# Kernel tuning notes

Measured on AMD Instinct MI355X. Metric: run time of the kernel, lower is better.

The kernel has to match this reference:

```python
import jax, jax.numpy as jnp
import numpy as np

EPS = 1e-5  # torch GroupNorm default
KNN_K = 16


def _knn_idx(Q, P, K):
    # Q:[B,Nq,3], P:[B,Np,3] -> idx [B,Nq,K], ascending squared distance
    d = (jnp.sum(Q * Q, -1)[:, :, None] + jnp.sum(P * P, -1)[:, None, :]
         - 2.0 * jnp.einsum('bqc,bkc->bqk', Q, P))
    _, idx = jax.lax.top_k(-d, K)
    return idx


def _gather_nbr(feat_bnc, idx_bqk):
    # feat:[B,Np,C], idx:[B,Nq,K] -> [B,Nq,K,C]  (knn_gather)
    return jax.vmap(lambda f, i: f[i])(feat_bnc, idx_bqk)


def _group_norm(x_bcnk, gamma, beta, num_groups=8):
    B, C, N, K = x_bcnk.shape
    G = min(num_groups, C)
    xg = x_bcnk.reshape(B, G, C // G, N, K)
    mu = xg.mean(axis=(2, 3, 4), keepdims=True)
    var = xg.var(axis=(2, 3, 4), keepdims=True)
    xn = ((xg - mu) / jnp.sqrt(var + EPS)).reshape(B, C, N, K)
    return xn * gamma[None, :, None, None] + beta[None, :, None, None]


def _edge_conv(Fq_bcn, Fk_bcn, Pq_b3n, Pk_b3n, k, W, gamma, beta):
    # EdgeConv: concat(x_j - x_i, x_i) -> conv1x1 -> GN -> ReLU -> max over K
    idx = _knn_idx(Pq_b3n.transpose(0, 2, 1), Pk_b3n.transpose(0, 2, 1), k)
    nbr = _gather_nbr(Fk_bcn.transpose(0, 2, 1), idx)          # [B,Nq,K,Cin]
    Fi = jnp.broadcast_to(Fq_bcn.transpose(0, 2, 1)[:, :, None, :], nbr.shape)
    pair = jnp.concatenate([nbr - Fi, Fi], axis=-1)            # [B,Nq,K,2Cin]
    out = jnp.einsum('oc,bnkc->bonk', W, pair)                 # conv 1x1, no bias
    out = _group_norm(out, gamma, beta)
    out = jax.nn.relu(out)
    return out.max(axis=-1)                                    # [B,Cout,Nq]


def _fps_idx(P_b3n, m):
    # Farthest point sampling starting at index 0 (pytorch3d default)
    def one(Pn3):
        d0 = jnp.sum((Pn3 - Pn3[0]) ** 2, -1)
        def step(dists, _):
            nxt = jnp.argmax(dists)
            d = jnp.sum((Pn3 - Pn3[nxt]) ** 2, -1)
            return jnp.minimum(dists, d), nxt
        _, idxs = jax.lax.scan(step, d0, None, length=m - 1)
        return jnp.concatenate([jnp.zeros((1,), jnp.int32), idxs.astype(jnp.int32)])
    return jax.vmap(one)(P_b3n.transpose(0, 2, 1))


def _gather_bcn(x_bcn, idx_bm):
    return jax.vmap(lambda x, i: x[:, i])(x_bcn, idx_bm)


def setup_inputs() -> dict:
    key = jax.random.key(0)
    ks = jax.random.split(key, 8)
    B, N = 2, 8192
    def w(k, shape, s=0.1):
        return jax.random.normal(k, shape, jnp.float32) * s
    return {
        'xyz': jax.random.normal(ks[0], (B, 3, N), jnp.float32),
        'stem_w': w(ks[1], (8, 3)), 'stem_b': jnp.zeros((8,), jnp.float32),
        'w1': w(ks[2], (32, 16)),  'g1': jnp.ones((32,), jnp.float32),  'b1': jnp.zeros((32,), jnp.float32),
        'w2': w(ks[3], (64, 64)),  'g2': jnp.ones((64,), jnp.float32),  'b2': jnp.zeros((64,), jnp.float32),
        'w3': w(ks[4], (64, 128)), 'g3': jnp.ones((64,), jnp.float32),  'b3': jnp.zeros((64,), jnp.float32),
        'w4': w(ks[5], (128, 128)),'g4': jnp.ones((128,), jnp.float32), 'b4': jnp.zeros((128,), jnp.float32),
    }


def reference(xyz, stem_w, stem_b, w1, g1, b1, w2, g2, b2, w3, g3, b3, w4, g4, b4):
    K = KNN_K
    P0 = xyz                                                     # [B,3,N0]
    F0 = jnp.einsum('oc,bcn->bon', stem_w, xyz) + stem_b[None, :, None]
    F0a = _edge_conv(F0, F0, P0, P0, K, w1, g1, b1)              # [B,32,N0]
    N0 = P0.shape[2]
    N1 = max(1, N0 // 4)
    idx1 = _fps_idx(P0, N1)
    P1 = _gather_bcn(P0, idx1)
    F1sk = _gather_bcn(F0a, idx1)
    F1a = _edge_conv(F1sk, F0a, P1, P0, K, w2, g2, b2)           # [B,64,N1]
    N2 = max(1, N1 // 4)
    idx2 = _fps_idx(P1, N2)
    P2 = _gather_bcn(P1, idx2)
    F2sk = _gather_bcn(F1a, idx2)
    F2mid = _edge_conv(F2sk, F1a, P2, P1, K, w3, g3, b3)         # [B,64,N2]
    F2a = _edge_conv(F2mid, F1a, P2, P1, K, w4, g4, b4)          # [B,128,N2]
    return (P0, F0a, P1, F1a, P2, F2a)
```

## Files before the change

kernel.cpp:

```cpp
#include <hip/hip_runtime.h>
#include <math.h>

typedef unsigned long long ull;

__global__ __launch_bounds__(256) void stem_fused(const float* __restrict__ xyz,
    const float* __restrict__ w, const float* __restrict__ bias,
    float* __restrict__ F0, float* __restrict__ P0o, int N){
  int id = blockIdx.x*256 + threadIdx.x;
  int n = id % N; int b = id / N;
  float x = xyz[((size_t)b*3+0)*N+n];
  float y = xyz[((size_t)b*3+1)*N+n];
  float z = xyz[((size_t)b*3+2)*N+n];
  P0o[((size_t)b*3+0)*N+n] = x;
  P0o[((size_t)b*3+1)*N+n] = y;
  P0o[((size_t)b*3+2)*N+n] = z;
  #pragma unroll
  for (int o=0;o<8;o++){
    float v = fmaf(w[o*3+0],x, fmaf(w[o*3+1],y, fmaf(w[o*3+2],z, bias[o])));
    F0[((size_t)b*8+o)*N+n] = v;
  }
}

__global__ __launch_bounds__(256) void knn_fused(
    const float* __restrict__ Pq, const float* __restrict__ Pp,
    int* __restrict__ idxk, int Nq, int Np){
  __shared__ float4 tile[4][256];
  __shared__ float  pd[16][4][64];
  __shared__ int    pi[16][4][64];
  int t = threadIdx.x, w = t>>6, l = t&63;
  int b = blockIdx.y;
  int qn = blockIdx.x*64 + l;
  const float* Pqb = Pq + (size_t)b*3*Nq;
  const float* Ppb = Pp + (size_t)b*3*Np;
  float qx = Pqb[qn], qy = Pqb[Nq+qn], qz = Pqb[2*Nq+qn];
  float qq = __fadd_rn(__fadd_rn(__fmul_rn(qx,qx),__fmul_rn(qy,qy)),__fmul_rn(qz,qz));

  float dl[16]; int il[16];
  #pragma unroll
  for (int u=0;u<16;u++){ dl[u]=INFINITY; il[u]=-1; }
  float maxd = INFINITY; int maxslot = 0;

  int CANDS = Np >> 2;
  int c0 = w*CANDS;
  for (int tb=0; tb<CANDS; tb+=256){
    __syncthreads();
    #pragma unroll
    for (int k=0;k<4;k++){
      int p = c0 + tb + k*64 + l;
      float px = Ppb[p], py = Ppb[Np+p], pz = Ppb[2*Np+p];
      float pp = __fadd_rn(__fadd_rn(__fmul_rn(px,px),__fmul_rn(py,py)),__fmul_rn(pz,pz));
      tile[w][k*64+l] = make_float4(px,py,pz,pp);
    }
    __syncthreads();
    for (int j=0;j<256;j++){
      float4 c = tile[w][j];
      float dot = __fadd_rn(__fadd_rn(__fmul_rn(qx,c.x),__fmul_rn(qy,c.y)),__fmul_rn(qz,c.z));
      float dc  = __fsub_rn(__fadd_rn(qq,c.w), __fmul_rn(2.0f,dot));
      if (dc < maxd){
        int pidx = c0 + tb + j;
        #pragma unroll
        for (int u=0;u<16;u++){ bool sel=(maxslot==u); dl[u]=sel?dc:dl[u]; il[u]=sel?pidx:il[u]; }
        maxd = dl[0]; maxslot = 0;
        #pragma unroll
        for (int u=1;u<16;u++){ bool g=(dl[u]>maxd); maxd=g?dl[u]:maxd; maxslot=g?u:maxslot; }
      }
    }
  }
  #pragma unroll
  for (int u=0;u<16;u++){ pd[u][w][l]=dl[u]; pi[u][w][l]=il[u]; }
  __syncthreads();
  if (t < 64){
    int q = t;
    float mdl[16]; int mil[16];
    #pragma unroll
    for (int u=0;u<16;u++){ mdl[u]=INFINITY; mil[u]=0x7fffffff; }
    float mmaxd = INFINITY; int mmaxi = 0x7fffffff; int mslot = 0;
    for (int s=0;s<4;s++){
      #pragma unroll
      for (int u=0;u<16;u++){
        float d = pd[u][s][q]; int ii = pi[u][s][q];
        bool better = (d < mmaxd) || (d == mmaxd && ii < mmaxi);
        if (better){
          #pragma unroll
          for (int v=0;v<16;v++){ bool sel=(mslot==v); mdl[v]=sel?d:mdl[v]; mil[v]=sel?ii:mil[v]; }
          mmaxd = mdl[0]; mmaxi = mil[0]; mslot = 0;
          #pragma unroll
          for (int v=1;v<16;v++){
            bool g = (mdl[v]>mmaxd) || (mdl[v]==mmaxd && mil[v]>mmaxi);
            mmaxd=g?mdl[v]:mmaxd; mmaxi=g?mil[v]:mmaxi; mslot=g?v:mslot;
          }
        }
      }
    }
    #pragma unroll
    for (int u=0;u<16;u++)
      idxk[((size_t)b*Nq + blockIdx.x*64 + q)*16 + u] = mil[u];
  }
}

template<int CIN, int COUT>
__global__ __launch_bounds__(1024) void edge_conv_pre(
    const float* __restrict__ Fk, const float* __restrict__ Fi,
    const int* __restrict__ idx, const float* __restrict__ W,
    float* __restrict__ pre, float* __restrict__ partS,
    float* __restrict__ partQ, int pstride, int Nq, int Np){
  constexpr int C2  = 2*CIN;
  constexpr int PAD = C2 + 4;
  constexpr int TO  = (COUT <= 64) ? COUT : 64;
  constexpr int OP  = COUT / TO;
  constexpr int CPG = COUT/8;
  constexpr int WPG = CPG/4;
  extern __shared__ float sm[];
  float* Wl = sm;
  float* Pl = sm + COUT*PAD;
  int t = threadIdx.x;
  int n = blockIdx.x, b = blockIdx.y;
  for (int e=t; e<COUT*C2; e += blockDim.x){
    int o=e/C2, c=e%C2; Wl[o*PAD+c] = W[e];
  }
  const int* idxn = idx + ((size_t)b*Nq + n)*16;
  for (int e=t; e<16*C2; e += blockDim.x){
    int k = e/C2, c = e%C2;
    int cc = (c < CIN) ? c : (c-CIN);
    float fi = Fi[((size_t)b*CIN + cc)*Nq + n];
    float v;
    if (c < CIN){ int nb = idxn[k]; v = Fk[((size_t)b*CIN + c)*Np + nb] - fi; }
    else v = fi;
    Pl[k*PAD+c] = v;
  }
  __syncthreads();
  int k = t & 15, o0 = t >> 4;
  float accv[OP];
  #pragma unroll
  for (int op=0; op<OP; op++){
    int o = o0 + op*TO;
    float acc = 0.f;
    #pragma unroll
    for (int c=0;c<C2;c+=4){
      float4 wv = *(const float4*)&Wl[o*PAD+c];
      float4 pv = *(const float4*)&Pl[k*PAD+c];
      acc = fmaf(wv.x,pv.x,acc); acc = fmaf(wv.y,pv.y,acc);
      acc = fmaf(wv.z,pv.z,acc); acc = fmaf(wv.w,pv.w,acc);
    }
    accv[op] = acc;
    pre[(((size_t)b*COUT + o)*Nq + n)*16 + k] = acc;
  }
  int w = t>>6;
  #pragma unroll
  for (int op=0; op<OP; op++){
    float s1 = accv[op], s2 = accv[op]*accv[op];
    #pragma unroll
    for (int off=32; off>=1; off>>=1){ s1 += __shfl_down(s1,off); s2 += __shfl_down(s2,off); }
    if ((t&63)==0){
      int o = o0 + op*TO;
      int g = o / CPG;
      int slot = n*WPG + (w % WPG);
      partS[((size_t)(b*8+g))*pstride + slot] = s1;
      partQ[((size_t)(b*8+g))*pstride + slot] = s2;
    }
  }
}

__global__ __launch_bounds__(256) void gn_combine(const float* __restrict__ partS,
    const float* __restrict__ partQ, float2* __restrict__ stats,
    int nslot, int pstride, double cnt){
  int bg = blockIdx.x, t = threadIdx.x;
  const float* ps = partS + (size_t)bg*pstride;
  const float* pq = partQ + (size_t)bg*pstride;
  double s=0.0, q=0.0;
  for (int i=t; i<nslot; i+=256){ s += (double)ps[i]; q += (double)pq[i]; }
  #pragma unroll
  for (int off=32; off>=1; off>>=1){ s += __shfl_down(s,off); q += __shfl_down(q,off); }
  __shared__ double ls[4], lq[4];
  int wid = t>>6;
  if ((t&63)==0){ ls[wid]=s; lq[wid]=q; }
  __syncthreads();
  if (t==0){
    double S=ls[0]+ls[1]+ls[2]+ls[3], Q=lq[0]+lq[1]+lq[2]+lq[3];
    double mu = S/cnt;
    double var = Q/cnt - mu*mu;
    stats[bg] = make_float2((float)mu, (float)(1.0/sqrt(var+1e-5)));
  }
}

template<int COUT>
__global__ __launch_bounds__(256) void gn_apply(const float* __restrict__ pre,
    const float2* __restrict__ stats, const float* __restrict__ gamma,
    const float* __restrict__ beta, float* __restrict__ outF, int Nq){
  int id = blockIdx.x*256 + threadIdx.x;
  int o = (id/Nq)%COUT; int b = id/(Nq*COUT);
  int g = o/(COUT/8);
  float2 st = stats[b*8+g];
  float muf = st.x, rstd = st.y;
  float ga=gamma[o], be=beta[o];
  const float4* p = (const float4*)(pre + (size_t)id*16);
  float m = 0.f;
  #pragma unroll
  for (int q=0;q<4;q++){
    float4 v = p[q];
    m = fmaxf(m, fmaf((v.x-muf)*rstd, ga, be));
    m = fmaxf(m, fmaf((v.y-muf)*rstd, ga, be));
    m = fmaxf(m, fmaf((v.z-muf)*rstd, ga, be));
    m = fmaxf(m, fmaf((v.w-muf)*rstd, ga, be));
  }
  outF[id] = m;
}

template<int COUT>
__global__ __launch_bounds__(1024) void gn_fused(const float* __restrict__ pre,
    const float* __restrict__ gamma, const float* __restrict__ beta,
    float* __restrict__ outF, int Nq){
  constexpr int CPG = COUT/8;
  int g = blockIdx.x, b = blockIdx.y, t = threadIdx.x;
  size_t base = (((size_t)b*COUT + g*CPG)*(size_t)Nq)*16;
  const float* p = pre + base;
  int len = CPG*Nq*16;
  double s=0.0, sq=0.0;
  for (int i = t*4; i < len; i += 4096){
    float4 v = *(const float4*)(p+i);
    s += (double)v.x; sq = fma((double)v.x,(double)v.x,sq);
    s += (double)v.y; sq = fma((double)v.y,(double)v.y,sq);
    s += (double)v.z; sq = fma((double)v.z,(double)v.z,sq);
    s += (double)v.w; sq = fma((double)v.w,(double)v.w,sq);
  }
  #pragma unroll
  for (int off=32; off>=1; off>>=1){ s += __shfl_down(s, off); sq += __shfl_down(sq, off); }
  __shared__ double ls[16], lq[16];
  __shared__ float stats[2];
  int wid = t>>6;
  if ((t&63)==0){ ls[wid]=s; lq[wid]=sq; }
  __syncthreads();
  if (t==0){
    double S=0.0, Q=0.0;
    #pragma unroll
    for (int w=0;w<16;w++){ S+=ls[w]; Q+=lq[w]; }
    double cnt = (double)CPG*(double)Nq*16.0;
    double mu  = S/cnt;
    double var = Q/cnt - mu*mu;
    stats[0] = (float)mu;
    stats[1] = (float)(1.0/sqrt(var+1e-5));
  }
  __syncthreads();
  float muf = stats[0], rstd = stats[1];
  int outs = CPG*Nq;
  for (int e=t; e<outs; e+=1024){
    int ol = e/Nq, n = e - ol*Nq;
    int o = g*CPG + ol;
    float ga = gamma[o], be = beta[o];
    const float4* pp = (const float4*)(p + (size_t)e*16);
    float m = 0.f;
    #pragma unroll
    for (int q=0;q<4;q++){
      float4 v = pp[q];
      m = fmaxf(m, fmaf((v.x-muf)*rstd, ga, be));
      m = fmaxf(m, fmaf((v.y-muf)*rstd, ga, be));
      m = fmaxf(m, fmaf((v.z-muf)*rstd, ga, be));
      m = fmaxf(m, fmaf((v.w-muf)*rstd, ga, be));
    }
    outF[((size_t)b*COUT + o)*Nq + n] = m;
  }
}

template<int CTRL>
__device__ __forceinline__ float dpp_maxf(float x){
  int y = __builtin_amdgcn_update_dpp(0, __float_as_int(x), CTRL, 0xf, 0xf, true);
  return fmaxf(x, __int_as_float(y));
}

template<int PPT, int BLK, int M>
__global__ __launch_bounds__(BLK, 2) void fps_kernel(const float* __restrict__ P,
    int* __restrict__ idx_out){
  constexpr int N  = PPT*BLK;
  constexpr int NW = BLK/64;
  extern __shared__ __align__(16) float sm[];
  float* lx = sm; float* ly = sm+N; float* lz = sm+2*N;
  ull* wk = (ull*)(sm + 3*N);
  int b = blockIdx.x, t = threadIdx.x;
  const float* Pb = P + (size_t)b*3*N;
  for (int i=t; i<N; i+=BLK){ lx[i]=Pb[i]; ly[i]=Pb[N+i]; lz[i]=Pb[2*N+i]; }
  __syncthreads();
  float px[PPT], py[PPT], pz[PPT], dist[PPT];
  #pragma unroll
  for (int j=0;j<PPT;j++){ int p=t*PPT+j; px[j]=lx[p]; py[j]=ly[p]; pz[j]=lz[p]; }
  #pragma unroll
  for (int j=0;j<PPT;j++){
    asm volatile("" : "+v"(px[j]), "+v"(py[j]), "+v"(pz[j]));
  }
  float sx = lx[0], sy = ly[0], sz = lz[0];
  float bd = -1.f; int bj = 0;
  #pragma unroll
  for (int j=0;j<PPT;j++){
    float dx=__fsub_rn(px[j],sx), dy=__fsub_rn(py[j],sy), dz=__fsub_rn(pz[j],sz);
    float dd=__fadd_rn(__fadd_rn(__fmul_rn(dx,dx),__fmul_rn(dy,dy)),__fmul_rn(dz,dz));
    dist[j]=dd;
    bool c = dd > bd; bd = c?dd:bd; bj = c?j:bj;
  }
  int pbest = t*PPT + bj;
  if (t==0) idx_out[(size_t)b*M] = 0;
  int wid = t>>6, lane = t&63, par = 0;
  for (int i=1;i<M;i++){
    float r = bd;
    r = dpp_maxf<0x111>(r); r = dpp_maxf<0x112>(r);
    r = dpp_maxf<0x114>(r); r = dpp_maxf<0x118>(r);
    r = dpp_maxf<0x142>(r); r = dpp_maxf<0x143>(r);
    float wmax = __int_as_float(__builtin_amdgcn_readlane(__float_as_int(r), 63));
    ull msk = __ballot(bd == wmax);
    int srcl = __ffsll(msk) - 1;
    int wp = __builtin_amdgcn_readlane(pbest, srcl);
    if (lane==0)
      wk[par*NW + wid] = ((ull)__float_as_uint(wmax)<<32)
                       | (unsigned)(~(unsigned)wp);
    __syncthreads();
    ull best = wk[par*NW];
    #pragma unroll
    for (int w=1;w<NW;w++){ ull o = wk[par*NW+w]; best = (o>best)?o:best; }
    unsigned widx = ~(unsigned)best;
    if (t==0) idx_out[(size_t)b*M + i] = (int)widx;
    float nsx = lx[widx], nsy = ly[widx], nsz = lz[widx];
    par ^= 1;
    float nbd = -1.f; int nbj = 0;
    #pragma unroll
    for (int j=0;j<PPT;j++){
      float dx=__fsub_rn(px[j],nsx), dy=__fsub_rn(py[j],nsy), dz=__fsub_rn(pz[j],nsz);
      float dd=__fadd_rn(__fadd_rn(__fmul_rn(dx,dx),__fmul_rn(dy,dy)),__fmul_rn(dz,dz));
      float nd = fminf(dist[j], dd);
      dist[j] = nd;
      bool c = nd > nbd; nbd = c?nd:nbd; nbj = c?j:nbj;
    }
    bd = nbd; pbest = t*PPT + nbj;
  }
}

__global__ __launch_bounds__(256) void gather_fused(float* __restrict__ Pdst,
    const float* __restrict__ Psrc, float* __restrict__ Fdst,
    const float* __restrict__ Fsrc, const int* __restrict__ idxv,
    int CF, int Nsrc, int M){
  int per = (3+CF)*M;
  int total = 2*per;
  for (int id = blockIdx.x*256 + threadIdx.x; id < total; id += gridDim.x*256){
    int b = id/per, r = id%per, c = r/M, m = r%M;
    int sn = idxv[(size_t)b*M + m];
    if (c < 3)
      Pdst[((size_t)b*3+c)*M+m] = Psrc[((size_t)b*3+c)*Nsrc+sn];
    else {
      int cf = c-3;
      Fdst[((size_t)b*CF+cf)*M+m] = Fsrc[((size_t)b*CF+cf)*Nsrc+sn];
    }
  }
}

extern "C" void kernel_launch(void* const* d_in, const int* in_sizes, int n_in,
                              void* d_out, int out_size, void* d_ws, size_t ws_size,
                              hipStream_t stream) {
  const float* xyz    = (const float*)d_in[0];
  const float* stem_w = (const float*)d_in[1];
  const float* stem_b = (const float*)d_in[2];
  const float* w1 = (const float*)d_in[3];
  const float* g1 = (const float*)d_in[4];
  const float* b1 = (const float*)d_in[5];
  const float* w2 = (const float*)d_in[6];
  const float* g2 = (const float*)d_in[7];
  const float* b2 = (const float*)d_in[8];
  const float* w3 = (const float*)d_in[9];
  const float* g3 = (const float*)d_in[10];
  const float* b3 = (const float*)d_in[11];
  const float* w4 = (const float*)d_in[12];
  const float* g4 = (const float*)d_in[13];
  const float* b4 = (const float*)d_in[14];

  float* out = (float*)d_out;
  float* P0o  = out + 0;
  float* F0a  = out + 49152;
  float* P1o  = out + 573440;
  float* F1a  = out + 585728;
  float* P2o  = out + 847872;
  float* F2a  = out + 850944;

  char* ws = (char*)d_ws;
  float* F0     = (float*)(ws + 0);
  float* pre    = (float*)(ws + 524288);
  int*   idxk   = (int*)  (ws + 34078720);
  float2* stats = (float2*)(ws + 35127296);
  int*   idx1   = (int*)  (ws + 35127424);
  int*   idx2   = (int*)  (ws + 35143808);
  float* F1sk   = (float*)(ws + 35147904);
  float* F2sk   = (float*)(ws + 35672192);
  float* F2mid  = (float*)(ws + 35934336);
  float* pS1 = (float*)(ws + 35147904);
  float* pQ1 = (float*)(ws + 35672192);
  float* pS2 = (float*)(ws + 17825792);
  float* pQ2 = (float*)(ws + 18087936);

  size_t smem_c1 = (size_t)(32*20  + 16*20 )*4;
  size_t smem_c2 = (size_t)(64*68  + 16*68 )*4;
  size_t smem_c3 = (size_t)(64*132 + 16*132)*4;
  size_t smem_c4 = (size_t)(128*132+ 16*132)*4;
  size_t smem_f1 = (size_t)3*8192*4 + 256;
  size_t smem_f2 = (size_t)3*2048*4 + 256;

  stem_fused<<<64, 256, 0, stream>>>(xyz, stem_w, stem_b, F0, P0o, 8192);
  knn_fused<<<dim3(128,2), 256, 0, stream>>>(xyz, xyz, idxk, 8192, 8192);
  edge_conv_pre<8,32><<<dim3(8192,2), 512, smem_c1, stream>>>(F0, F0, idxk, w1, pre, pS1, pQ1, 8192, 8192, 8192);
  gn_combine<<<16, 256, 0, stream>>>(pS1, pQ1, stats, 8192, 8192, 524288.0);
  gn_apply<32><<<2048, 256, 0, stream>>>(pre, stats, g1, b1, F0a, 8192);

  fps_kernel<16,512,2048><<<2, 512, smem_f1, stream>>>(xyz, idx1);
  gather_fused<<<560, 256, 0, stream>>>(P1o, xyz, F1sk, F0a, idx1, 32, 8192, 2048);

  knn_fused<<<dim3(32,2), 256, 0, stream>>>(P1o, xyz, idxk, 2048, 8192);
  edge_conv_pre<32,64><<<dim3(2048,2), 1024, smem_c2, stream>>>(F0a, F1sk, idxk, w2, pre, pS2, pQ2, 4096, 2048, 8192);
  gn_combine<<<16, 256, 0, stream>>>(pS2, pQ2, stats, 4096, 4096, 262144.0);
  gn_apply<64><<<1024, 256, 0, stream>>>(pre, stats, g2, b2, F1a, 2048);

  fps_kernel<4,512,512><<<2, 512, smem_f2, stream>>>(P1o, idx2);
  gather_fused<<<268, 256, 0, stream>>>(P2o, P1o, F2sk, F1a, idx2, 64, 2048, 512);

  knn_fused<<<dim3(8,2), 256, 0, stream>>>(P2o, P1o, idxk, 512, 2048);
  edge_conv_pre<64,64><<<dim3(512,2), 1024, smem_c3, stream>>>(F1a, F2sk, idxk, w3, pre, pS2, pQ2, 4096, 512, 2048);
  gn_fused<64><<<dim3(8,2), 1024, 0, stream>>>(pre, g3, b3, F2mid, 512);

  edge_conv_pre<64,128><<<dim3(512,2), 1024, smem_c4, stream>>>(F1a, F2mid, idxk, w4, pre, pS2, pQ2, 4096, 512, 2048);
  gn_fused<128><<<dim3(8,2), 1024, 0, stream>>>(pre, g4, b4, F2a, 512);

  (void)in_sizes; (void)n_in; (void)out_size; (void)ws_size;
}
```

Measured before the change: 3.609 ms.

## Run FPS concurrently with stem and KNN in merged heterogeneous launches

Merges farthest-point sampling, the stem projection and the first-level KNN into one launch where block ids pick the role, and does the same for the second FPS with the second KNN. The serial FPS scan, which uses only two blocks, now runs alongside the parallel KNN work instead of after it. FPS now uses 256-thread blocks with twice the points per thread, which lengthens each block's serial loop. Every block of the merged kernels reserves the large FPS shared-memory allocation, which may limit KNN occupancy.

```diff
diff --git a/kernel.cpp b/kernel.cpp
--- a/kernel.cpp
+++ b/kernel.cpp
@@ -3,33 +3,83 @@
 
 typedef unsigned long long ull;
 
-__global__ __launch_bounds__(256) void stem_fused(const float* __restrict__ xyz,
-    const float* __restrict__ w, const float* __restrict__ bias,
-    float* __restrict__ F0, float* __restrict__ P0o, int N){
-  int id = blockIdx.x*256 + threadIdx.x;
-  int n = id % N; int b = id / N;
-  float x = xyz[((size_t)b*3+0)*N+n];
-  float y = xyz[((size_t)b*3+1)*N+n];
-  float z = xyz[((size_t)b*3+2)*N+n];
-  P0o[((size_t)b*3+0)*N+n] = x;
-  P0o[((size_t)b*3+1)*N+n] = y;
-  P0o[((size_t)b*3+2)*N+n] = z;
-  #pragma unroll
-  for (int o=0;o<8;o++){
-    float v = fmaf(w[o*3+0],x, fmaf(w[o*3+1],y, fmaf(w[o*3+2],z, bias[o])));
-    F0[((size_t)b*8+o)*N+n] = v;
-  }
-}
-
-__global__ __launch_bounds__(256) void knn_fused(
-    const float* __restrict__ Pq, const float* __restrict__ Pp,
-    int* __restrict__ idxk, int Nq, int Np){
-  __shared__ float4 tile[4][256];
-  __shared__ float  pd[16][4][64];
-  __shared__ int    pi[16][4][64];
+template<int CTRL>
+__device__ __forceinline__ float dpp_maxf(float x){
+  int y = __builtin_amdgcn_update_dpp(0, __float_as_int(x), CTRL, 0xf, 0xf, true);
+  return fmaxf(x, __int_as_float(y));
+}
+
+template<int PPT, int BLK, int M>
+__device__ void fps_body(const float* __restrict__ P, int* __restrict__ idx_out,
+                         int b, float* sm){
+  constexpr int N  = PPT*BLK;
+  constexpr int NW = BLK/64;
+  float* lx = sm; float* ly = sm+N; float* lz = sm+2*N;
+  ull* wk = (ull*)(sm + 3*N);
+  int t = threadIdx.x;
+  const float* Pb = P + (size_t)b*3*N;
+  for (int i=t; i<N; i+=BLK){ lx[i]=Pb[i]; ly[i]=Pb[N+i]; lz[i]=Pb[2*N+i]; }
+  __syncthreads();
+  float px[PPT], py[PPT], pz[PPT], dist[PPT];
+  #pragma unroll
+  for (int j=0;j<PPT;j++){ int p=t*PPT+j; px[j]=lx[p]; py[j]=ly[p]; pz[j]=lz[p]; }
+  #pragma unroll
+  for (int j=0;j<PPT;j++){
+    asm volatile("" : "+v"(px[j]), "+v"(py[j]), "+v"(pz[j]));
+  }
+  float sx = lx[0], sy = ly[0], sz = lz[0];
+  float bd = -1.f; int bj = 0;
+  #pragma unroll
+  for (int j=0;j<PPT;j++){
+    float dx=__fsub_rn(px[j],sx), dy=__fsub_rn(py[j],sy), dz=__fsub_rn(pz[j],sz);
+    float dd=__fadd_rn(__fadd_rn(__fmul_rn(dx,dx),__fmul_rn(dy,dy)),__fmul_rn(dz,dz));
+    dist[j]=dd;
+    bool c = dd > bd; bd = c?dd:bd; bj = c?j:bj;
+  }
+  int pbest = t*PPT + bj;
+  if (t==0) idx_out[(size_t)b*M] = 0;
+  int wid = t>>6, lane = t&63, par = 0;
+  for (int i=1;i<M;i++){
+    float r = bd;
+    r = dpp_maxf<0x111>(r); r = dpp_maxf<0x112>(r);
+    r = dpp_maxf<0x114>(r); r = dpp_maxf<0x118>(r);
+    r = dpp_maxf<0x142>(r); r = dpp_maxf<0x143>(r);
+    float wmax = __int_as_float(__builtin_amdgcn_readlane(__float_as_int(r), 63));
+    ull msk = __ballot(bd == wmax);
+    int srcl = __ffsll(msk) - 1;
+    int wp = __builtin_amdgcn_readlane(pbest, srcl);
+    if (lane==0)
+      wk[par*NW + wid] = ((ull)__float_as_uint(wmax)<<32)
+                       | (unsigned)(~(unsigned)wp);
+    __syncthreads();
+    ull best = wk[par*NW];
+    #pragma unroll
+    for (int w=1;w<NW;w++){ ull o = wk[par*NW+w]; best = (o>best)?o:best; }
+    unsigned widx = ~(unsigned)best;
+    if (t==0) idx_out[(size_t)b*M + i] = (int)widx;
+    float nsx = lx[widx], nsy = ly[widx], nsz = lz[widx];
+    par ^= 1;
+    float nbd = -1.f; int nbj = 0;
+    #pragma unroll
+    for (int j=0;j<PPT;j++){
+      float dx=__fsub_rn(px[j],nsx), dy=__fsub_rn(py[j],nsy), dz=__fsub_rn(pz[j],nsz);
+      float dd=__fadd_rn(__fadd_rn(__fmul_rn(dx,dx),__fmul_rn(dy,dy)),__fmul_rn(dz,dz));
+      float nd = fminf(dist[j], dd);
+      dist[j] = nd;
+      bool c = nd > nbd; nbd = c?nd:nbd; nbj = c?j:nbj;
+    }
+    bd = nbd; pbest = t*PPT + nbj;
+  }
+}
+
+__device__ void knn_body(const float* __restrict__ Pq, const float* __restrict__ Pp,
+                         int* __restrict__ idxk, int Nq, int Np, int qb, int b,
+                         float* smbase){
+  float4* tile = (float4*)smbase;
+  float*  pd   = smbase + 4096;
+  int*    pi   = (int*)(smbase + 8192);
   int t = threadIdx.x, w = t>>6, l = t&63;
-  int b = blockIdx.y;
-  int qn = blockIdx.x*64 + l;
+  int qn = qb*64 + l;
   const float* Pqb = Pq + (size_t)b*3*Nq;
   const float* Ppb = Pp + (size_t)b*3*Np;
   float qx = Pqb[qn], qy = Pqb[Nq+qn], qz = Pqb[2*Nq+qn];
@@ -49,11 +99,11 @@
       int p = c0 + tb + k*64 + l;
       float px = Ppb[p], py = Ppb[Np+p], pz = Ppb[2*Np+p];
       float pp = __fadd_rn(__fadd_rn(__fmul_rn(px,px),__fmul_rn(py,py)),__fmul_rn(pz,pz));
-      tile[w][k*64+l] = make_float4(px,py,pz,pp);
+      tile[w*256 + k*64 + l] = make_float4(px,py,pz,pp);
     }
     __syncthreads();
     for (int j=0;j<256;j++){
-      float4 c = tile[w][j];
+      float4 c = tile[w*256 + j];
       float dot = __fadd_rn(__fadd_rn(__fmul_rn(qx,c.x),__fmul_rn(qy,c.y)),__fmul_rn(qz,c.z));
       float dc  = __fsub_rn(__fadd_rn(qq,c.w), __fmul_rn(2.0f,dot));
       if (dc < maxd){
@@ -67,7 +117,7 @@
     }
   }
   #pragma unroll
-  for (int u=0;u<16;u++){ pd[u][w][l]=dl[u]; pi[u][w][l]=il[u]; }
+  for (int u=0;u<16;u++){ pd[(u*4+w)*64 + l]=dl[u]; pi[(u*4+w)*64 + l]=il[u]; }
   __syncthreads();
   if (t < 64){
     int q = t;
@@ -78,7 +128,7 @@
     for (int s=0;s<4;s++){
       #pragma unroll
       for (int u=0;u<16;u++){
-        float d = pd[u][s][q]; int ii = pi[u][s][q];
+        float d = pd[(u*4+s)*64 + q]; int ii = pi[(u*4+s)*64 + q];
         bool better = (d < mmaxd) || (d == mmaxd && ii < mmaxi);
         if (better){
           #pragma unroll
@@ -94,8 +144,55 @@
     }
     #pragma unroll
     for (int u=0;u<16;u++)
-      idxk[((size_t)b*Nq + blockIdx.x*64 + q)*16 + u] = mil[u];
-  }
+      idxk[((size_t)b*Nq + qb*64 + q)*16 + u] = mil[u];
+  }
+}
+
+__global__ __launch_bounds__(256, 1) void mega_a(const float* __restrict__ xyz,
+    const float* __restrict__ sw, const float* __restrict__ sb,
+    float* __restrict__ F0, float* __restrict__ P0o,
+    int* __restrict__ idxk, int* __restrict__ idx1){
+  extern __shared__ __align__(16) float sm[];
+  int bid = blockIdx.x;
+  if (bid < 2){
+    fps_body<32,256,2048>(xyz, idx1, bid, sm);
+  } else if (bid < 66){
+    int id = (bid-2)*256 + threadIdx.x;
+    int n = id & 8191, b = id >> 13;
+    float x = xyz[((size_t)b*3+0)*8192+n];
+    float y = xyz[((size_t)b*3+1)*8192+n];
+    float z = xyz[((size_t)b*3+2)*8192+n];
+    P0o[((size_t)b*3+0)*8192+n] = x;
+    P0o[((size_t)b*3+1)*8192+n] = y;
+    P0o[((size_t)b*3+2)*8192+n] = z;
+    #pragma unroll
+    for (int o=0;o<8;o++){
+      float v = fmaf(sw[o*3+0],x, fmaf(sw[o*3+1],y, fmaf(sw[o*3+2],z, sb[o])));
+      F0[((size_t)b*8+o)*8192+n] = v;
+    }
+  } else {
+    int r = bid - 66;
+    knn_body(xyz, xyz, idxk, 8192, 8192, r & 127, r >> 7, sm);
+  }
+}
+
+__global__ __launch_bounds__(256, 1) void mega_b(const float* __restrict__ P1o,
+    const float* __restrict__ xyz, int* __restrict__ idxk, int* __restrict__ idx2){
+  extern __shared__ __align__(16) float sm[];
+  int bid = blockIdx.x;
+  if (bid < 2){
+    fps_body<8,256,512>(P1o, idx2, bid, sm);
+  } else {
+    int r = bid - 2;
+    knn_body(P1o, xyz, idxk, 2048, 8192, r & 31, r >> 5, sm);
+  }
+}
+
+__global__ __launch_bounds__(256) void knn_fused(
+    const float* __restrict__ Pq, const float* __restrict__ Pp,
+    int* __restrict__ idxk, int Nq, int Np){
+  __shared__ __align__(16) float smk[12288];
+  knn_body(Pq, Pp, idxk, Nq, Np, blockIdx.x, blockIdx.y, smk);
 }
 
 template<int CIN, int COUT>
@@ -261,76 +358,6 @@
   }
 }
 
-template<int CTRL>
-__device__ __forceinline__ float dpp_maxf(float x){
-  int y = __builtin_amdgcn_update_dpp(0, __float_as_int(x), CTRL, 0xf, 0xf, true);
-  return fmaxf(x, __int_as_float(y));
-}
-
-template<int PPT, int BLK, int M>
-__global__ __launch_bounds__(BLK, 2) void fps_kernel(const float* __restrict__ P,
-    int* __restrict__ idx_out){
-  constexpr int N  = PPT*BLK;
-  constexpr int NW = BLK/64;
-  extern __shared__ __align__(16) float sm[];
-  float* lx = sm; float* ly = sm+N; float* lz = sm+2*N;
-  ull* wk = (ull*)(sm + 3*N);
-  int b = blockIdx.x, t = threadIdx.x;
-  const float* Pb = P + (size_t)b*3*N;
-  for (int i=t; i<N; i+=BLK){ lx[i]=Pb[i]; ly[i]=Pb[N+i]; lz[i]=Pb[2*N+i]; }
-  __syncthreads();
-  float px[PPT], py[PPT], pz[PPT], dist[PPT];
-  #pragma unroll
-  for (int j=0;j<PPT;j++){ int p=t*PPT+j; px[j]=lx[p]; py[j]=ly[p]; pz[j]=lz[p]; }
-  #pragma unroll
-  for (int j=0;j<PPT;j++){
-    asm volatile("" : "+v"(px[j]), "+v"(py[j]), "+v"(pz[j]));
-  }
-  float sx = lx[0], sy = ly[0], sz = lz[0];
-  float bd = -1.f; int bj = 0;
-  #pragma unroll
-  for (int j=0;j<PPT;j++){
-    float dx=__fsub_rn(px[j],sx), dy=__fsub_rn(py[j],sy), dz=__fsub_rn(pz[j],sz);
-    float dd=__fadd_rn(__fadd_rn(__fmul_rn(dx,dx),__fmul_rn(dy,dy)),__fmul_rn(dz,dz));
-    dist[j]=dd;
-    bool c = dd > bd; bd = c?dd:bd; bj = c?j:bj;
-  }
-  int pbest = t*PPT + bj;
-  if (t==0) idx_out[(size_t)b*M] = 0;
-  int wid = t>>6, lane = t&63, par = 0;
-  for (int i=1;i<M;i++){
-    float r = bd;
-    r = dpp_maxf<0x111>(r); r = dpp_maxf<0x112>(r);
-    r = dpp_maxf<0x114>(r); r = dpp_maxf<0x118>(r);
-    r = dpp_maxf<0x142>(r); r = dpp_maxf<0x143>(r);
-    float wmax = __int_as_float(__builtin_amdgcn_readlane(__float_as_int(r), 63));
-    ull msk = __ballot(bd == wmax);
-    int srcl = __ffsll(msk) - 1;
-    int wp = __builtin_amdgcn_readlane(pbest, srcl);
-    if (lane==0)
-      wk[par*NW + wid] = ((ull)__float_as_uint(wmax)<<32)
-                       | (unsigned)(~(unsigned)wp);
-    __syncthreads();
-    ull best = wk[par*NW];
-    #pragma unroll
-    for (int w=1;w<NW;w++){ ull o = wk[par*NW+w]; best = (o>best)?o:best; }
-    unsigned widx = ~(unsigned)best;
-    if (t==0) idx_out[(size_t)b*M + i] = (int)widx;
-    float nsx = lx[widx], nsy = ly[widx], nsz = lz[widx];
-    par ^= 1;
-    float nbd = -1.f; int nbj = 0;
-    #pragma unroll
-    for (int j=0;j<PPT;j++){
-      float dx=__fsub_rn(px[j],nsx), dy=__fsub_rn(py[j],nsy), dz=__fsub_rn(pz[j],nsz);
-      float dd=__fadd_rn(__fadd_rn(__fmul_rn(dx,dx),__fmul_rn(dy,dy)),__fmul_rn(dz,dz));
-      float nd = fminf(dist[j], dd);
-      dist[j] = nd;
-      bool c = nd > nbd; nbd = c?nd:nbd; nbj = c?j:nbj;
-    }
-    bd = nbd; pbest = t*PPT + nbj;
-  }
-}
-
 __global__ __launch_bounds__(256) void gather_fused(float* __restrict__ Pdst,
     const float* __restrict__ Psrc, float* __restrict__ Fdst,
     const float* __restrict__ Fsrc, const int* __restrict__ idxv,
@@ -395,24 +422,21 @@
   size_t smem_c2 = (size_t)(64*68  + 16*68 )*4;
   size_t smem_c3 = (size_t)(64*132 + 16*132)*4;
   size_t smem_c4 = (size_t)(128*132+ 16*132)*4;
-  size_t smem_f1 = (size_t)3*8192*4 + 256;
-  size_t smem_f2 = (size_t)3*2048*4 + 256;
-
-  stem_fused<<<64, 256, 0, stream>>>(xyz, stem_w, stem_b, F0, P0o, 8192);
-  knn_fused<<<dim3(128,2), 256, 0, stream>>>(xyz, xyz, idxk, 8192, 8192);
+  size_t smem_ma = (size_t)3*8192*4 + 256;
+  size_t smem_mb = (size_t)49152 + 256;
+
+  mega_a<<<322, 256, smem_ma, stream>>>(xyz, stem_w, stem_b, F0, P0o, idxk, idx1);
+
   edge_conv_pre<8,32><<<dim3(8192,2), 512, smem_c1, stream>>>(F0, F0, idxk, w1, pre, pS1, pQ1, 8192, 8192, 8192);
   gn_combine<<<16, 256, 0, stream>>>(pS1, pQ1, stats, 8192, 8192, 524288.0);
   gn_apply<32><<<2048, 256, 0, stream>>>(pre, stats, g1, b1, F0a, 8192);
-
-  fps_kernel<16,512,2048><<<2, 512, smem_f1, stream>>>(xyz, idx1);
   gather_fused<<<560, 256, 0, stream>>>(P1o, xyz, F1sk, F0a, idx1, 32, 8192, 2048);
 
-  knn_fused<<<dim3(32,2), 256, 0, stream>>>(P1o, xyz, idxk, 2048, 8192);
+  mega_b<<<66, 256, smem_mb, stream>>>(P1o, xyz, idxk, idx2);
+
   edge_conv_pre<32,64><<<dim3(2048,2), 1024, smem_c2, stream>>>(F0a, F1sk, idxk, w2, pre, pS2, pQ2, 4096, 2048, 8192);
   gn_combine<<<16, 256, 0, stream>>>(pS2, pQ2, stats, 4096, 4096, 262144.0);
   gn_apply<64><<<1024, 256, 0, stream>>>(pre, stats, g2, b2, F1a, 2048);
-
-  fps_kernel<4,512,512><<<2, 512, smem_f2, stream>>>(P1o, idx2);
   gather_fused<<<268, 256, 0, stream>>>(P2o, P1o, F2sk, F1a, idx2, 64, 2048, 512);
 
   knn_fused<<<dim3(8,2), 256, 0, stream>>>(P2o, P1o, idxk, 512, 2048);
```

New measurement: 3.290 ms. 1.1x faster.
